# Kernel tuning notes

Measured on AMD Instinct MI355X. Metric: run time of the kernel, lower is better.

The kernel has to match this reference:

```python
import jax, jax.numpy as jnp
import numpy as np

C = 64      # in_channels
H = 32      # hidden_size per direction
K = 8       # kernel_size
L = 4       # num_layers
EPS = 1e-5


def _sru_dir(x, W, v, b, reverse):
    # x: (T, N, in); one SRU direction.
    if reverse:
        x = x[::-1]
    U = x @ W                                   # (T, N, 4H): [candidate z, f_pre, r_pre, highway x']
    z, fp, rp, xp = jnp.split(U, 4, axis=-1)
    vf, vr = jnp.split(v, 2)
    bf, br = jnp.split(b, 2)

    def step(c, inp):
        z_t, fp_t, rp_t, xp_t = inp
        f = jax.nn.sigmoid(fp_t + vf * c + bf)
        r = jax.nn.sigmoid(rp_t + vr * c + br)
        c_new = f * c + (1.0 - f) * z_t
        h = r * c_new + (1.0 - r) * xp_t
        return c_new, h

    c0 = jnp.zeros((x.shape[1], H), x.dtype)
    _, h = jax.lax.scan(step, c0, (z, fp, rp, xp))
    if reverse:
        h = h[::-1]
    return h


def _sru(x, W0, Wr, v, b):
    # Bidirectional multi-layer SRU. x: (T, N, C*K) -> (T, N, 2H)
    Ws = [W0] + [Wr[i] for i in range(Wr.shape[0])]
    h = x
    for l in range(L):
        hf = _sru_dir(h, Ws[l][0], v[l, 0], b[l, 0], False)
        hb = _sru_dir(h, Ws[l][1], v[l, 1], b[l, 1], True)
        h = jnp.concatenate([hf, hb], axis=-1)
    return h


def setup_inputs() -> dict:
    key = jax.random.key(0)
    ks = jax.random.split(key, 8)
    B, Fdim, Tdim = 2, 128, 250
    s = 0.05
    x = jax.random.normal(ks[0], (B, C, Fdim, Tdim), jnp.float32)
    gamma = jnp.ones((C,), jnp.float32)
    beta = jnp.zeros((C,), jnp.float32)
    W0 = jax.random.normal(ks[1], (2, C * K, 4 * H), jnp.float32) * s       # layer 0, 2 dirs
    Wr = jax.random.normal(ks[2], (L - 1, 2, 2 * H, 4 * H), jnp.float32) * s  # layers 1..3
    v = jax.random.normal(ks[3], (L, 2, 2 * H), jnp.float32) * s            # recurrent gate vectors
    b = jnp.zeros((L, 2, 2 * H), jnp.float32)                               # gate biases
    wct = jax.random.normal(ks[4], (2 * H, C, K), jnp.float32) * s          # ConvTranspose1d (in,out,k)
    bct = jnp.zeros((C,), jnp.float32)
    return {"x": x, "gamma": gamma, "beta": beta, "W0": W0, "Wr": Wr,
            "v": v, "b": b, "wct": wct, "bct": bct}


def reference(x, gamma, beta, W0, Wr, v, b, wct, bct):
    x = jnp.swapaxes(x, -1, -2)                 # [B, C, T, F]
    res = x
    B, Cc, T, F = x.shape
    # GroupNorm(num_groups=1): normalize over (C,T,F) per sample, per-channel affine.
    mean = jnp.mean(x, axis=(1, 2, 3), keepdims=True)
    var = jnp.var(x, axis=(1, 2, 3), keepdims=True)
    xn = (x - mean) * jax.lax.rsqrt(var + EPS)
    xn = xn * gamma[None, :, None, None] + beta[None, :, None, None]
    # -> (B*F, C, T), then unfold over T with window K (channel-major block layout).
    xu = jnp.transpose(xn, (0, 3, 1, 2)).reshape(B * F, Cc, T)
    Tn = T - K + 1
    win = jnp.stack([xu[:, :, k:k + Tn] for k in range(K)], axis=2)   # (N, C, K, Tn)
    win = win.reshape(B * F, Cc * K, Tn)
    s = jnp.transpose(win, (2, 0, 1))           # (Tn, N, C*K)
    h = _sru(s, W0, Wr, v, b)                   # (Tn, N, 2H)
    y = jnp.transpose(h, (1, 2, 0))             # (N, 2H, Tn)
    # ConvTranspose1d stride 1 == full correlation with flipped kernel.
    w_conv = jnp.transpose(wct, (1, 0, 2))[:, :, ::-1]                # (out, in, k)
    y = jax.lax.conv_general_dilated(y, w_conv, (1,), [(K - 1, K - 1)],
                                     dimension_numbers=("NCH", "OIH", "NCH"))
    y = y + bct[None, :, None]                  # (N, C, T)
    y = y.reshape(B, F, Cc, T)
    y = jnp.transpose(y, (0, 2, 3, 1))          # [B, C, T, F]
    y = y + res
    return jnp.swapaxes(y, -1, -2)              # back to [B, C, F, T]
```

## Files before the change

### kernel.cpp

```cpp
#include <hip/hip_runtime.h>
#include <math.h>

#define Tt 250
#define TnN 243
#define Nn 256
#define EPS_ 1e-5f
#define LOG2E 1.44269504f

typedef unsigned short u16;
typedef __bf16 bf16x8 __attribute__((ext_vector_type(8)));
typedef __bf16 bf16x4 __attribute__((ext_vector_type(4)));
typedef float f32x4 __attribute__((ext_vector_type(4)));

__device__ __forceinline__ u16 f2bf(float f) {
    unsigned u = __builtin_bit_cast(unsigned, f);
    u += 0x7FFFu + ((u >> 16) & 1u);
    return (u16)(u >> 16);
}
__device__ __forceinline__ float bf2f(u16 s) {
    unsigned u = ((unsigned)s) << 16;
    return __builtin_bit_cast(float, u);
}
__device__ __forceinline__ float hw_exp2(float x) {
    return __builtin_amdgcn_exp2f(x);
}

__device__ __forceinline__ void async_load16(const void* g, void* l) {
    __builtin_amdgcn_global_load_lds(
        (const __attribute__((address_space(1))) unsigned int*)g,
        (__attribute__((address_space(3))) unsigned int*)l, 16, 0, 0);
}

__device__ __forceinline__ void dma72g(const u16* gsrc, int rstride, u16* ldst, int nseg,
                                       int w, int lane, int nw) {
    for (int seg = w; seg < nseg; seg += nw) {
        int c9 = seg * 64 + lane;
        int row = c9 / 9, sub = c9 - row * 9;
        const u16* src = (sub < 8) ? &gsrc[row * rstride + sub * 8] : gsrc;
        async_load16(src, ldst + seg * 512);
    }
}

template<int D>
__device__ __forceinline__ void chain_run(u16* Zr, u16* Fr, float kf, float bf_) {
    bf16x8 z8 = *(const bf16x8*)&Zr[D ? 240 : 0];
    bf16x8 f8 = *(const bf16x8*)&Fr[D ? 240 : 0];
    float c = 0.f;
    for (int grp = 0; grp < 31; ++grp) {
        int gb = D ? (30 - grp) * 8 : grp * 8;
        bf16x8 zn = z8, fn = f8;
        if (grp < 30) {
            int gbn = D ? (29 - grp) * 8 : (grp + 1) * 8;
            zn = *(const bf16x8*)&Zr[gbn];
            fn = *(const bf16x8*)&Fr[gbn];
        }
        bf16x8 co;
        #pragma unroll
        for (int k = 0; k < 8; ++k) {
            const int idx = D ? (7 - k) : k;
            int t = gb + idx;
            float uz = (float)z8[idx];
            float af = -LOG2E * ((float)f8[idx] + bf_);
            float xe = fmaf(kf, c, af);
            float fg = __builtin_amdgcn_rcpf(1.f + hw_exp2(xe));
            float cn = fmaf(fg, c - uz, uz);
            bool ok = (t < TnN);
            if (ok) c = cn;
            co[idx] = ok ? (__bf16)c : (__bf16)0.f;
        }
        *(bf16x8*)&Zr[gb] = co;
        z8 = zn; f8 = fn;
    }
}

__global__ __launch_bounds__(256) void k_stats(const float* __restrict__ x,
                                               float* __restrict__ stats) {
    __shared__ float ls[4], ls2[4];
    const int sb = blockIdx.x, tid = threadIdx.x;
    const int b = sb >> 7;
    const float4* xb = (const float4*)(x + (size_t)b * 64 * 128 * Tt);
    const int n4 = 64 * 128 * Tt / 4;
    float s = 0.f, s2 = 0.f;
    for (int i = (sb & 127) * 256 + tid; i < n4; i += 128 * 256) {
        float4 vv = xb[i];
        s  += vv.x + vv.y + vv.z + vv.w;
        s2 += vv.x * vv.x + vv.y * vv.y + vv.z * vv.z + vv.w * vv.w;
    }
    for (int off = 32; off; off >>= 1) {
        s  += __shfl_down(s, off);
        s2 += __shfl_down(s2, off);
    }
    int lane = tid & 63, w = tid >> 6;
    if (lane == 0) { ls[w] = s; ls2[w] = s2; }
    __syncthreads();
    if (tid == 0) {
        float a = 0.f, a2 = 0.f;
        for (int i = 0; i < 4; i++) { a += ls[i]; a2 += ls2[i]; }
        stats[sb * 2]     = a;
        stats[sb * 2 + 1] = a2;
    }
}

__global__ __launch_bounds__(512) void k_norm(const float* __restrict__ x, const float* __restrict__ stats,
                       const float* __restrict__ gamma, const float* __restrict__ beta,
                       const float* __restrict__ W0, const float* __restrict__ Wr,
                       const float* __restrict__ wct,
                       u16* __restrict__ xbt, u16* __restrict__ W0k,
                       u16* __restrict__ Wrt, u16* __restrict__ Wcto) {
    __shared__ u16 lt[64 * 260];
    __shared__ float sm2[2];
    const int n = blockIdx.x, tid = threadIdx.x;
    const int b = n >> 7, f = n & 127;
    if (tid < 64) {
        float a = 0.f, a2 = 0.f;
        #pragma unroll
        for (int p = 0; p < 2; ++p) {
            int sb = b * 128 + tid + p * 64;
            a  += stats[sb * 2];
            a2 += stats[sb * 2 + 1];
        }
        for (int off = 32; off; off >>= 1) {
            a  += __shfl_down(a, off);
            a2 += __shfl_down(a2, off);
        }
        if (tid == 0) { sm2[0] = a; sm2[1] = a2; }
    }
    #pragma unroll
    for (int it = 0; it < 2; ++it) {
        int idx = it * 131072 + n * 512 + tid;
        if (idx < 131072) {
            int k = idx >> 14, j = (idx >> 6) & 255, c = idx & 63;
            int d = j >> 7, ck = c * 8 + k;
            W0k[idx] = f2bf(W0[((size_t)d * 512 + ck) * 128 + (j & 127)]);
        } else if (idx < 180224) {
            int r = idx - 131072;
            int i = r & 63, j = (r >> 6) & 255, lidx = r >> 14;
            Wrt[r] = f2bf(Wr[(size_t)(lidx * 2 + (j >> 7)) * 8192 + i * 128 + (j & 127)]);
        } else if (idx < 212992) {
            int r = idx - 180224;
            int o = r >> 9; int k = r & 511; int kk = k >> 6, ci = k & 63;
            Wcto[r] = f2bf(wct[(size_t)ci * 512 + o * 8 + kk]);
        }
    }
    __syncthreads();
    const float inv = 1.0f / (float)(64 * 128 * Tt);
    float mean = sm2[0] * inv;
    float var  = sm2[1] * inv - mean * mean;
    float rstd = rsqrtf(var + EPS_);
    const int c = tid >> 3, vq = tid & 7;
    const float gm = gamma[c] * rstd;
    const float bt = beta[c] - mean * gm;
    const float* xr = x + ((size_t)(b * 64 + c) * 128 + f) * Tt;
    #pragma unroll
    for (int j = 0; j < 16; ++j) {
        int t0 = vq * 2 + j * 16;
        unsigned pv = 0u;
        if (t0 < Tt) {
            float2 xv = *(const float2*)&xr[t0];
            pv = (unsigned)f2bf(fmaf(xv.x, gm, bt)) | ((unsigned)f2bf(fmaf(xv.y, gm, bt)) << 16);
        }
        *(unsigned*)&lt[c * 260 + t0] = pv;
    }
    __syncthreads();
    const int cg = tid & 7, tq = tid >> 3;
    #pragma unroll
    for (int it = 0; it < 4; ++it) {
        int t = it * 64 + tq;
        u16 tmp[8];
        #pragma unroll
        for (int jj = 0; jj < 8; ++jj) tmp[jj] = lt[(cg * 8 + jj) * 260 + t];
        uint4 o;
        o.x = (unsigned)tmp[0] | ((unsigned)tmp[1] << 16);
        o.y = (unsigned)tmp[2] | ((unsigned)tmp[3] << 16);
        o.z = (unsigned)tmp[4] | ((unsigned)tmp[5] << 16);
        o.w = (unsigned)tmp[6] | ((unsigned)tmp[7] << 16);
        *(uint4*)&xbt[(size_t)n * 16384 + t * 64 + cg * 8] = o;
    }
}

#define HS0 0
#define ZT0 19008
#define FT0 35136
#define BM0 51264
#define SH_U16 81856
__global__ __launch_bounds__(1024) void k_tail(const u16* __restrict__ XbT,
                                               const u16* __restrict__ W0k,
                                               const u16* __restrict__ Wrt,
                                               const u16* __restrict__ Wc,
                                               const float* __restrict__ v,
                                               const float* __restrict__ bbias,
                                               const float* __restrict__ bct,
                                               const float* __restrict__ x,
                                               float* __restrict__ out) {
    __shared__ __align__(16) u16 sh[SH_U16];
    u16* Hs = sh + HS0;
    u16* ZT = sh + ZT0;
    u16* FT = sh + FT0;
    u16* Bm = sh + BM0;
    const int tid = threadIdx.x;
    const int n = blockIdx.x;
    const int lane = tid & 63, w = tid >> 6;
    const int ml = lane & 15, q = lane >> 4;
    const int wm = w >> 1, wn = w & 1;
    const int b = n >> 7, f = n & 127;

    for (int lay = 0; lay < 4; ++lay) {
        f32x4 acc[2][8];
        #pragma unroll
        for (int mt = 0; mt < 2; ++mt)
            #pragma unroll
            for (int nt = 0; nt < 8; ++nt) acc[mt][nt] = (f32x4){0.f, 0.f, 0.f, 0.f};

        if (lay == 0) {
            const u16* Xn = XbT + (size_t)n * 16384;
            u16* Bb0 = sh + ZT0;
            u16* Bb1 = Bm;
            dma72g(Xn, 64, Hs, 36, w, lane, 16);
            dma72g(W0k, 64, Bb0, 36, w, lane, 16);
            __syncthreads();
            #pragma unroll
            for (int k = 0; k < 8; ++k) {
                u16* Bl = (k & 1) ? Bb1 : Bb0;
                if (k < 7)
                    dma72g(W0k + (size_t)(k + 1) * 16384, 64, (k & 1) ? Bb0 : Bb1, 36, w, lane, 16);
                #pragma unroll
                for (int c2 = 0; c2 < 2; ++c2) {
                    int c0 = c2 * 32;
                    bf16x8 af[2];
                    #pragma unroll
                    for (int mt = 0; mt < 2; ++mt)
                        af[mt] = *(const bf16x8*)&Hs[(wm * 32 + mt * 16 + ml + k) * 72 + c0 + q * 8];
                    #pragma unroll
                    for (int nt = 0; nt < 8; ++nt) {
                        bf16x8 bfr = *(const bf16x8*)&Bl[(wn * 128 + nt * 16 + ml) * 72 + c0 + q * 8];
                        #pragma unroll
                        for (int mt = 0; mt < 2; ++mt)
                            acc[mt][nt] = __builtin_amdgcn_mfma_f32_16x16x32_bf16(af[mt], bfr, acc[mt][nt], 0, 0, 0);
                    }
                }
                __syncthreads();
            }
        } else {
            #pragma unroll
            for (int c2 = 0; c2 < 2; ++c2) {
                int c0 = c2 * 32;
                bf16x8 af[2];
                #pragma unroll
                for (int mt = 0; mt < 2; ++mt)
                    af[mt] = *(const bf16x8*)&Hs[(wm * 32 + mt * 16 + ml + 7) * 72 + c0 + q * 8];
                #pragma unroll
                for (int nt = 0; nt < 8; ++nt) {
                    bf16x8 bfr = *(const bf16x8*)&Bm[(wn * 128 + nt * 16 + ml) * 72 + c0 + q * 8];
                    #pragma unroll
                    for (int mt = 0; mt < 2; ++mt)
                        acc[mt][nt] = __builtin_amdgcn_mfma_f32_16x16x32_bf16(af[mt], bfr, acc[mt][nt], 0, 0, 0);
                }
            }
        }

        #pragma unroll
        for (int mt = 0; mt < 2; ++mt) {
            int t0 = wm * 32 + mt * 16 + q * 4;
            if (t0 < TnN) {
                bool vec = (t0 + 4 <= TnN);
                #pragma unroll
                for (int nt = 0; nt < 4; ++nt) {
                    int g2 = nt >> 1, hh = (nt & 1) * 16 + ml;
                    u16* P = (g2 ? FT : ZT) + (wn * 32 + hh) * 252;
                    if (vec) {
                        uint2 pv;
                        pv.x = (unsigned)f2bf(acc[mt][nt][0]) | ((unsigned)f2bf(acc[mt][nt][1]) << 16);
                        pv.y = (unsigned)f2bf(acc[mt][nt][2]) | ((unsigned)f2bf(acc[mt][nt][3]) << 16);
                        *(uint2*)&P[t0] = pv;
                    } else {
                        #pragma unroll
                        for (int r = 0; r < 4; ++r) {
                            int t = t0 + r;
                            if (t < TnN) P[t] = f2bf(acc[mt][nt][r]);
                        }
                    }
                }
            }
        }
        __syncthreads();

        if (lay < 3) {
            dma72g(Wrt + (size_t)lay * 16384, 64, Bm, 36, w, lane, 16);
        } else {
            #pragma unroll
            for (int i = 0; i < 4; ++i)
                dma72g(Wc + i * 64, 512, Bm + i * 4608, 9, w, lane, 16);
        }

        const float* vv = v + (size_t)(lay * 2) * 64;
        const float* bv = bbias + (size_t)(lay * 2) * 64;

        if (w < 2 && lane < 32) {
            const int d = w, h = lane;
            const float vf = vv[d * 64 + h], bf_ = bv[d * 64 + h];
            const float kf = -LOG2E * vf;
            u16* Zr = &ZT[(d * 32 + h) * 252];
            u16* Fr = &FT[(d * 32 + h) * 252];
            if (d == 0) chain_run<0>(Zr, Fr, kf, bf_);
            else        chain_run<1>(Zr, Fr, kf, bf_);
        }
        __syncthreads();

        if (lay == 0) {
            for (int i = tid; i < 21 * 72; i += 1024) {
                int r = i / 72, ci = i - r * 72;
                int row = r < 7 ? r : (TnN + r);
                Hs[row * 72 + ci] = 0;
            }
        }
        #pragma unroll
        for (int mt = 0; mt < 2; ++mt) {
            int t0 = wm * 32 + mt * 16 + q * 4;
            if (t0 < TnN) {
                #pragma unroll
                for (int hi = 0; hi < 2; ++hi) {
                    int hh = hi * 16 + ml;
                    float vr_ = vv[wn * 64 + 32 + hh], br_ = bv[wn * 64 + 32 + hh];
                    float kr = -LOG2E * vr_;
                    const u16* Cr = &ZT[(wn * 32 + hh) * 252];
                    bf16x4 c4 = *(const bf16x4*)&Cr[t0];
                    float ct[4];
                    #pragma unroll
                    for (int r = 0; r < 4; ++r) ct[r] = (float)c4[r];
                    float cprv[4];
                    if (wn == 0) {
                        cprv[0] = (t0 == 0) ? 0.f : bf2f(Cr[t0 - 1]);
                        cprv[1] = ct[0]; cprv[2] = ct[1]; cprv[3] = ct[2];
                    } else {
                        cprv[0] = ct[1]; cprv[1] = ct[2]; cprv[2] = ct[3];
                        cprv[3] = bf2f(Cr[t0 + 4]);
                    }
                    f32x4 rp = acc[mt][4 + hi];
                    f32x4 xp = acc[mt][6 + hi];
                    #pragma unroll
                    for (int r = 0; r < 4; ++r) {
                        int t = t0 + r;
                        if (t < TnN) {
                            float cpr = cprv[r];
                            if (wn == 1 && t == TnN - 1) cpr = 0.f;
                            float xr = fmaf(kr, cpr, -LOG2E * (rp[r] + br_));
                            float rg = __builtin_amdgcn_rcpf(1.f + hw_exp2(xr));
                            float hv = fmaf(rg, ct[r] - xp[r], xp[r]);
                            Hs[(t + 7) * 72 + wn * 32 + hh] = f2bf(hv);
                        }
                    }
                }
            }
        }
        __syncthreads();
    }

    {
        u16* T47 = sh + ZT0;
        float* Cf = (float*)(sh + 37440);
        const int tc0 = w * 16 + q * 4;
        f32x4 cacc[4] = {};
        #pragma unroll
        for (int i = 0; i < 4; ++i)
            dma72g(Wc + (4 + i) * 64, 512, T47 + i * 4608, 9, w, lane, 16);
        #pragma unroll
        for (int m = 0; m < 8; ++m) {
            if (m == 4) __syncthreads();
            const u16* Bl = (m < 4) ? (Bm + m * 4608) : (T47 + (m - 4) * 4608);
            #pragma unroll
            for (int c2 = 0; c2 < 2; ++c2) {
                int ci0 = c2 * 32;
                bf16x8 af = *(const bf16x8*)&Hs[(w * 16 + ml - m + 7) * 72 + ci0 + q * 8];
                #pragma unroll
                for (int nt = 0; nt < 4; ++nt) {
                    bf16x8 bfv = *(const bf16x8*)&Bl[(nt * 16 + ml) * 72 + ci0 + q * 8];
                    cacc[nt] = __builtin_amdgcn_mfma_f32_16x16x32_bf16(af, bfv, cacc[nt], 0, 0, 0);
                }
            }
        }
        __syncthreads();
        float bc[4];
        #pragma unroll
        for (int nt = 0; nt < 4; ++nt) bc[nt] = bct[nt * 16 + ml];
        #pragma unroll
        for (int r = 0; r < 4; ++r) {
            int t = tc0 + r;
            if (t < Tt) {
                #pragma unroll
                for (int nt = 0; nt < 4; ++nt)
                    Cf[t * 68 + nt * 16 + ml] = cacc[nt][r] + bc[nt];
            }
        }
        __syncthreads();
        {
            const int sub = tid & 15;
            const int o = tid >> 4;
            const float* xrow = x + ((size_t)(b * 64 + o) * 128 + f) * Tt;
            float* orow = out + ((size_t)(b * 64 + o) * 128 + f) * Tt;
            #pragma unroll
            for (int it = 0; it < 8; ++it) {
                int j = it * 32 + sub * 2;
                if (j < Tt) {
                    float2 xv = *(const float2*)&xrow[j];
                    float2 ov;
                    ov.x = Cf[j * 68 + o] + xv.x;
                    ov.y = Cf[(j + 1) * 68 + o] + xv.y;
                    *(float2*)&orow[j] = ov;
                }
            }
        }
    }
}

extern "C" void kernel_launch(void* const* d_in, const int* in_sizes, int n_in,
                              void* d_out, int out_size, void* d_ws, size_t ws_size,
                              hipStream_t stream) {
    (void)in_sizes; (void)n_in; (void)out_size; (void)ws_size;
    const float* x     = (const float*)d_in[0];
    const float* gamma = (const float*)d_in[1];
    const float* beta  = (const float*)d_in[2];
    const float* W0    = (const float*)d_in[3];
    const float* Wr    = (const float*)d_in[4];
    const float* v     = (const float*)d_in[5];
    const float* bb    = (const float*)d_in[6];
    const float* wct   = (const float*)d_in[7];
    const float* bct   = (const float*)d_in[8];
    float* out = (float*)d_out;

    char* base = (char*)d_ws;
    float* stats = (float*)base;
    u16* W0k  = (u16*)(base + 4096);
    u16* Wrt  = (u16*)(base + 4096 + 262144);
    u16* Wcto = (u16*)(base + 4096 + 262144 + 98304);
    u16* XbT  = (u16*)(base + 4096 + 262144 + 98304 + 65536);

    k_stats<<<dim3(256), 256, 0, stream>>>(x, stats);
    k_norm<<<dim3(256), 512, 0, stream>>>(x, stats, gamma, beta, W0, Wr, wct,
                                          XbT, W0k, Wrt, Wcto);
    k_tail<<<dim3(256), 1024, 0, stream>>>(XbT, W0k, Wrt, Wcto, v, bb, bct, x, out);
}
```

Before: 174.4 us.

## Fuse stats reduction into norm kernel with grid-wide atomic barrier

Removes the separate k_stats launch. Each k_norm block now computes partial sums over its own slice of x, publishes them with atomics, and spins on a per-batch counter until all 128 blocks for that batch have arrived. Only then does it compute mean and variance and normalize. This saves one kernel launch and a second pass over x, but it adds a memset, relies on all 256 blocks being co-resident for the spin barrier, and adds spin latency.

```diff
diff --git a/kernel.cpp b/kernel.cpp
--- a/kernel.cpp
+++ b/kernel.cpp
@@ -73,64 +73,53 @@
     }
 }
 
-__global__ __launch_bounds__(256) void k_stats(const float* __restrict__ x,
-                                               float* __restrict__ stats) {
-    __shared__ float ls[4], ls2[4];
-    const int sb = blockIdx.x, tid = threadIdx.x;
-    const int b = sb >> 7;
-    const float4* xb = (const float4*)(x + (size_t)b * 64 * 128 * Tt);
-    const int n4 = 64 * 128 * Tt / 4;
-    float s = 0.f, s2 = 0.f;
-    for (int i = (sb & 127) * 256 + tid; i < n4; i += 128 * 256) {
-        float4 vv = xb[i];
-        s  += vv.x + vv.y + vv.z + vv.w;
-        s2 += vv.x * vv.x + vv.y * vv.y + vv.z * vv.z + vv.w * vv.w;
-    }
-    for (int off = 32; off; off >>= 1) {
-        s  += __shfl_down(s, off);
-        s2 += __shfl_down(s2, off);
-    }
-    int lane = tid & 63, w = tid >> 6;
-    if (lane == 0) { ls[w] = s; ls2[w] = s2; }
-    __syncthreads();
-    if (tid == 0) {
-        float a = 0.f, a2 = 0.f;
-        for (int i = 0; i < 4; i++) { a += ls[i]; a2 += ls2[i]; }
-        stats[sb * 2]     = a;
-        stats[sb * 2 + 1] = a2;
-    }
-}
-
-__global__ __launch_bounds__(512) void k_norm(const float* __restrict__ x, const float* __restrict__ stats,
+__global__ __launch_bounds__(512) void k_norm(const float* __restrict__ x,
                        const float* __restrict__ gamma, const float* __restrict__ beta,
                        const float* __restrict__ W0, const float* __restrict__ Wr,
                        const float* __restrict__ wct,
+                       float* __restrict__ stats, unsigned* __restrict__ cnt,
                        u16* __restrict__ xbt, u16* __restrict__ W0k,
                        u16* __restrict__ Wrt, u16* __restrict__ Wcto) {
     __shared__ u16 lt[64 * 260];
-    __shared__ float sm2[2];
+    __shared__ float ls[8], ls2[8], sm2[2];
     const int n = blockIdx.x, tid = threadIdx.x;
     const int b = n >> 7, f = n & 127;
-    if (tid < 64) {
-        float a = 0.f, a2 = 0.f;
-        #pragma unroll
-        for (int p = 0; p < 2; ++p) {
-            int sb = b * 128 + tid + p * 64;
-            a  += stats[sb * 2];
-            a2 += stats[sb * 2 + 1];
+    const int c = tid >> 3, vq = tid & 7;
+    const float* xr = x + ((size_t)(b * 64 + c) * 128 + f) * Tt;
+
+    {
+        float s = 0.f, s2 = 0.f;
+        #pragma unroll
+        for (int j = 0; j < 16; ++j) {
+            int t0 = vq * 2 + j * 16;
+            if (t0 < Tt) {
+                float2 xv = *(const float2*)&xr[t0];
+                s  += xv.x + xv.y;
+                s2 += xv.x * xv.x + xv.y * xv.y;
+            }
         }
         for (int off = 32; off; off >>= 1) {
-            a  += __shfl_down(a, off);
-            a2 += __shfl_down(a2, off);
-        }
-        if (tid == 0) { sm2[0] = a; sm2[1] = a2; }
-    }
+            s  += __shfl_down(s, off);
+            s2 += __shfl_down(s2, off);
+        }
+        int lane = tid & 63, w = tid >> 6;
+        if (lane == 0) { ls[w] = s; ls2[w] = s2; }
+        __syncthreads();
+        if (tid == 0) {
+            float a = 0.f, a2 = 0.f;
+            for (int i = 0; i < 8; i++) { a += ls[i]; a2 += ls2[i]; }
+            __hip_atomic_store(&stats[n * 2],     a,  __ATOMIC_RELAXED, __HIP_MEMORY_SCOPE_AGENT);
+            __hip_atomic_store(&stats[n * 2 + 1], a2, __ATOMIC_RELAXED, __HIP_MEMORY_SCOPE_AGENT);
+            __hip_atomic_fetch_add(&cnt[b], 1u, __ATOMIC_RELEASE, __HIP_MEMORY_SCOPE_AGENT);
+        }
+    }
+
     #pragma unroll
     for (int it = 0; it < 2; ++it) {
         int idx = it * 131072 + n * 512 + tid;
         if (idx < 131072) {
-            int k = idx >> 14, j = (idx >> 6) & 255, c = idx & 63;
-            int d = j >> 7, ck = c * 8 + k;
+            int k = idx >> 14, j = (idx >> 6) & 255, cc = idx & 63;
+            int d = j >> 7, ck = cc * 8 + k;
             W0k[idx] = f2bf(W0[((size_t)d * 512 + ck) * 128 + (j & 127)]);
         } else if (idx < 180224) {
             int r = idx - 131072;
@@ -142,15 +131,33 @@
             Wcto[r] = f2bf(wct[(size_t)ci * 512 + o * 8 + kk]);
         }
     }
+
+    if (tid == 0) {
+        while (__hip_atomic_load(&cnt[b], __ATOMIC_ACQUIRE, __HIP_MEMORY_SCOPE_AGENT) < 128u) {}
+    }
     __syncthreads();
+    if (tid < 64) {
+        float a = 0.f, a2 = 0.f;
+        #pragma unroll
+        for (int p = 0; p < 2; ++p) {
+            int sb = b * 128 + tid + p * 64;
+            a  += __hip_atomic_load(&stats[sb * 2],     __ATOMIC_RELAXED, __HIP_MEMORY_SCOPE_AGENT);
+            a2 += __hip_atomic_load(&stats[sb * 2 + 1], __ATOMIC_RELAXED, __HIP_MEMORY_SCOPE_AGENT);
+        }
+        for (int off = 32; off; off >>= 1) {
+            a  += __shfl_down(a, off);
+            a2 += __shfl_down(a2, off);
+        }
+        if (tid == 0) { sm2[0] = a; sm2[1] = a2; }
+    }
+    __syncthreads();
+
     const float inv = 1.0f / (float)(64 * 128 * Tt);
     float mean = sm2[0] * inv;
     float var  = sm2[1] * inv - mean * mean;
     float rstd = rsqrtf(var + EPS_);
-    const int c = tid >> 3, vq = tid & 7;
     const float gm = gamma[c] * rstd;
     const float bt = beta[c] - mean * gm;
-    const float* xr = x + ((size_t)(b * 64 + c) * 128 + f) * Tt;
     #pragma unroll
     for (int j = 0; j < 16; ++j) {
         int t0 = vq * 2 + j * 16;
@@ -429,13 +436,14 @@
 
     char* base = (char*)d_ws;
     float* stats = (float*)base;
+    unsigned* cnt = (unsigned*)(base + 2048);
     u16* W0k  = (u16*)(base + 4096);
     u16* Wrt  = (u16*)(base + 4096 + 262144);
     u16* Wcto = (u16*)(base + 4096 + 262144 + 98304);
     u16* XbT  = (u16*)(base + 4096 + 262144 + 98304 + 65536);
 
-    k_stats<<<dim3(256), 256, 0, stream>>>(x, stats);
-    k_norm<<<dim3(256), 512, 0, stream>>>(x, stats, gamma, beta, W0, Wr, wct,
-                                          XbT, W0k, Wrt, Wcto);
+    hipMemsetAsync(cnt, 0, 8, stream);
+    k_norm<<<dim3(256), 512, 0, stream>>>(x, gamma, beta, W0, Wr, wct,
+                                          stats, cnt, XbT, W0k, Wrt, Wcto);
     k_tail<<<dim3(256), 1024, 0, stream>>>(XbT, W0k, Wrt, Wcto, v, bb, bct, x, out);
 }
```

New measurement: 184.6 us. 1.06x slower.
